# Kernel tuning notes

Measured on AMD Instinct MI355X. Metric: run time of the kernel, lower is better.

The kernel has to match this reference:

```python
import jax, jax.numpy as jnp
import numpy as np

B, S, D, H = 2, 2048, 1024, 16
DH = D // H
MASK_FACTOR = -10000.0
EPS = 1e-6


def setup_inputs() -> dict:
    key = jax.random.key(0)
    ks = jax.random.split(key, 12)
    sc = 1.0 / np.sqrt(D)
    inp = {
        'query': jax.random.normal(ks[0], (B, S, D), jnp.float32),
        'key':   jax.random.normal(ks[1], (B, S, D), jnp.float32),
        'value': jax.random.normal(ks[2], (B, S, D), jnp.float32),
        # mask: 1.0 = masked position (causal), shape (B, 1, Sq, Sk)
        'mask': jnp.broadcast_to(
            (1.0 - jnp.tril(jnp.ones((S, S), jnp.float32)))[None, None], (B, 1, S, S)
        ),
        'wq_w': jax.random.normal(ks[3], (D, D), jnp.float32) * sc,
        'wq_b': jnp.zeros((D,), jnp.float32),
        'wk_w': jax.random.normal(ks[4], (D, D), jnp.float32) * sc,
        'wk_b': jnp.zeros((D,), jnp.float32),
        'wv_w': jax.random.normal(ks[5], (D, D), jnp.float32) * sc,
        'wv_b': jnp.zeros((D,), jnp.float32),
        'wo_w': jax.random.normal(ks[6], (D, D), jnp.float32) * sc,
        'wo_b': jnp.zeros((D,), jnp.float32),
        'ln_g': jnp.ones((D,), jnp.float32),
        'ln_b': jnp.zeros((D,), jnp.float32),
    }
    return inp


def _split_heads(x):
    # (B, S, D) -> (B, H, S, DH)
    b, s, _ = x.shape
    return x.reshape(b, s, H, DH).transpose(0, 2, 1, 3)


def _layer_norm(x, g, b):
    mu = jnp.mean(x, axis=-1, keepdims=True)
    var = jnp.mean(jnp.square(x - mu), axis=-1, keepdims=True)
    return (x - mu) * jax.lax.rsqrt(var + EPS) * g + b


def reference(query, key, value, mask, wq_w, wq_b, wk_w, wk_b, wv_w, wv_b,
              wo_w, wo_b, ln_g, ln_b):
    q = _split_heads(query @ wq_w + wq_b)
    k = _split_heads(key @ wk_w + wk_b)
    v = _split_heads(value @ wv_w + wv_b)

    logits = jnp.einsum('bhqd,bhkd->bhqk', q, k) / jnp.sqrt(jnp.float32(DH))
    logits = logits * (1.0 - mask) + mask * MASK_FACTOR
    attn = jax.nn.softmax(logits, axis=-1)  # (B, H, Sq, Sk)

    ctx = jnp.einsum('bhqk,bhkd->bhqd', attn, v)
    ctx = ctx.transpose(0, 2, 1, 3).reshape(query.shape[0], -1, D)

    out = ctx @ wo_w + wo_b
    out = out + query  # residual
    out = _layer_norm(out, ln_g, ln_b)
    return out, attn
```

## Files before the change

kernel.cpp:

```cpp
#include <hip/hip_runtime.h>

#define B_ 2
#define S_ 2048
#define D_ 1024
#define H_ 16
#define DH_ 64
#define EPS_ 1e-6f

typedef short bf16x8 __attribute__((ext_vector_type(8)));
typedef float f32x4  __attribute__((ext_vector_type(4)));

__device__ __forceinline__ ushort f2bf(float x) {
    uint u = __float_as_uint(x);
    return (ushort)((u + 0x7fffu + ((u >> 16) & 1u)) >> 16);
}
__device__ __forceinline__ float bf2f(ushort h) {
    return __uint_as_float(((uint)h) << 16);
}
__device__ __forceinline__ void split_bf(float x, ushort& hi, ushort& lo) {
    hi = f2bf(x);
    lo = f2bf(x - bf2f(hi));
}

__global__ __launch_bounds__(256) void prep_weights_kernel(
    const float* __restrict__ w0, const float* __restrict__ w1,
    const float* __restrict__ w2, const float* __restrict__ w3,
    ushort* __restrict__ Wth, ushort* __restrict__ Wtl)
{
    const int wi = blockIdx.z;
    const float* W = (wi == 0) ? w0 : (wi == 1) ? w1 : (wi == 2) ? w2 : w3;
    ushort* th = Wth + (size_t)wi * D_ * D_;
    ushort* tl = Wtl + (size_t)wi * D_ * D_;
    const int k0 = blockIdx.x * 32, n0 = blockIdx.y * 32;
    const int tid = threadIdx.x;
    __shared__ float t[32][33];
#pragma unroll
    for (int l = 0; l < 4; ++l) {
        int idx = tid + l * 256;
        int kk = idx >> 5, nn = idx & 31;
        t[kk][nn] = W[(size_t)(k0 + kk) * D_ + n0 + nn];
    }
    __syncthreads();
#pragma unroll
    for (int l = 0; l < 4; ++l) {
        int idx = tid + l * 256;
        int nn = idx >> 5, kk = idx & 31;
        ushort h, lo;
        split_bf(t[kk][nn], h, lo);
        th[(size_t)(n0 + nn) * D_ + k0 + kk] = h;
        tl[(size_t)(n0 + nn) * D_ + k0 + kk] = lo;
    }
}

template <int MODE>
__device__ __forceinline__ void gemm_mfma_body(
    const float* __restrict__ A, const ushort* __restrict__ Bh,
    const ushort* __restrict__ Bl, const float* __restrict__ bias,
    const float* __restrict__ residual, float* __restrict__ Cf,
    ushort* __restrict__ Ch, ushort* __restrict__ Cl,
    int M, int N, int K, int bx, int by)
{
    __shared__ ushort Ah[128][40];
    __shared__ ushort Al[128][40];

    const int tid = threadIdx.x;
    const int lane = tid & 63, w = tid >> 6;
    const int l15 = lane & 15, l4 = lane >> 4;
    const int row0 = by * 128, col0 = bx * 128;
    const int wm = (w >> 1) * 64, wn = (w & 1) * 64;

    const f32x4 zf = {0.f, 0.f, 0.f, 0.f};
    f32x4 acc[4][4];
#pragma unroll
    for (int i = 0; i < 4; ++i)
#pragma unroll
        for (int j = 0; j < 4; ++j) acc[i][j] = zf;

    for (int k0 = 0; k0 < K; k0 += 32) {
#pragma unroll
        for (int l = 0; l < 4; ++l) {
            int idx = tid + l * 256;
            int r = idx >> 3, c4 = (idx & 7) * 4;
            const float4 a = *(const float4*)&A[(size_t)(row0 + r) * K + k0 + c4];
            ushort h0, h1, h2, h3, q0, q1, q2, q3;
            split_bf(a.x, h0, q0); split_bf(a.y, h1, q1);
            split_bf(a.z, h2, q2); split_bf(a.w, h3, q3);
            *(ushort4*)&Ah[r][c4] = make_ushort4(h0, h1, h2, h3);
            *(ushort4*)&Al[r][c4] = make_ushort4(q0, q1, q2, q3);
        }
        bf16x8 bh_[4], bl_[4];
#pragma unroll
        for (int j = 0; j < 4; ++j) {
            const size_t bo = (size_t)(col0 + wn + j * 16 + l15) * K + k0 + l4 * 8;
            bh_[j] = *(const bf16x8*)&Bh[bo];
            bl_[j] = *(const bf16x8*)&Bl[bo];
        }
        __syncthreads();
        bf16x8 ah_[4], al_[4];
#pragma unroll
        for (int i = 0; i < 4; ++i) {
            ah_[i] = *(const bf16x8*)&Ah[wm + i * 16 + l15][l4 * 8];
            al_[i] = *(const bf16x8*)&Al[wm + i * 16 + l15][l4 * 8];
        }
#pragma unroll
        for (int i = 0; i < 4; ++i)
#pragma unroll
            for (int j = 0; j < 4; ++j) {
                acc[i][j] = __builtin_amdgcn_mfma_f32_16x16x32_bf16(
                    ah_[i], bh_[j], acc[i][j], 0, 0, 0);
                acc[i][j] = __builtin_amdgcn_mfma_f32_16x16x32_bf16(
                    ah_[i], bl_[j], acc[i][j], 0, 0, 0);
                acc[i][j] = __builtin_amdgcn_mfma_f32_16x16x32_bf16(
                    al_[i], bh_[j], acc[i][j], 0, 0, 0);
            }
        __syncthreads();
    }

#pragma unroll
    for (int i = 0; i < 4; ++i) {
#pragma unroll
        for (int j = 0; j < 4; ++j) {
            const int col = col0 + wn + j * 16 + l15;
            const float bb = bias[col];
            const int mbase = row0 + wm + i * 16 + l4 * 4;
            if (MODE == 0) {
#pragma unroll
                for (int e = 0; e < 4; ++e) {
                    const int m = mbase + e;
                    float v = acc[i][j][e] + bb;
                    if (residual) v += residual[(size_t)m * N + col];
                    Cf[(size_t)m * N + col] = v;
                }
            } else if (MODE == 1) {
#pragma unroll
                for (int e = 0; e < 4; ++e) {
                    const int m = mbase + e;
                    ushort h, lo;
                    split_bf(acc[i][j][e] + bb, h, lo);
                    Ch[(size_t)m * N + col] = h;
                    Cl[(size_t)m * N + col] = lo;
                }
            } else {
                const int bb_ = mbase / S_;
                const int s0 = mbase - bb_ * S_;
                const int hh = col >> 6, dh = col & 63;
                ushort hv[4], lv[4];
#pragma unroll
                for (int e = 0; e < 4; ++e)
                    split_bf(acc[i][j][e] + bb, hv[e], lv[e]);
                const size_t ofs =
                    (((size_t)bb_ * H_ + hh) * DH_ + dh) * S_ + s0;
                *(ushort4*)&Ch[ofs] = make_ushort4(hv[0], hv[1], hv[2], hv[3]);
                *(ushort4*)&Cl[ofs] = make_ushort4(lv[0], lv[1], lv[2], lv[3]);
            }
        }
    }
}

__global__ __launch_bounds__(256) void gemm_qkv_mfma(
    const float* __restrict__ q, const float* __restrict__ k,
    const float* __restrict__ v,
    const ushort* __restrict__ Wth, const ushort* __restrict__ Wtl,
    const float* __restrict__ bq, const float* __restrict__ bk,
    const float* __restrict__ bv,
    ushort* __restrict__ Qh, ushort* __restrict__ Ql,
    ushort* __restrict__ Kh, ushort* __restrict__ Kl,
    ushort* __restrict__ Vth, ushort* __restrict__ Vtl)
{
    const int z = blockIdx.z;
    const size_t wofs = (size_t)z * D_ * D_;
    if (z == 0)
        gemm_mfma_body<1>(q, Wth, Wtl, bq, nullptr, nullptr, Qh, Ql,
                          B_ * S_, D_, D_, blockIdx.x, blockIdx.y);
    else if (z == 1)
        gemm_mfma_body<1>(k, Wth + wofs, Wtl + wofs, bk, nullptr, nullptr,
                          Kh, Kl, B_ * S_, D_, D_, blockIdx.x, blockIdx.y);
    else
        gemm_mfma_body<2>(v, Wth + wofs, Wtl + wofs, bv, nullptr, nullptr,
                          Vth, Vtl, B_ * S_, D_, D_, blockIdx.x, blockIdx.y);
}

__global__ __launch_bounds__(256) void gemm_out_mfma(
    const float* __restrict__ ctx, const ushort* __restrict__ Wth,
    const ushort* __restrict__ Wtl, const float* __restrict__ bias,
    const float* __restrict__ residual, float* __restrict__ pre)
{
    gemm_mfma_body<0>(ctx, Wth, Wtl, bias, residual, pre, nullptr, nullptr,
                      B_ * S_, D_, D_, blockIdx.x, blockIdx.y);
}

__global__ __launch_bounds__(256) void qk_mfma_kernel(
    const ushort* __restrict__ Qh, const ushort* __restrict__ Ql,
    const ushort* __restrict__ Kh, const ushort* __restrict__ Kl,
    float* __restrict__ logits)
{
    const int tk = blockIdx.x, tq = blockIdx.y;
    if (tk > tq) return;
    const int bh = blockIdx.z, b = bh >> 4, h = bh & 15;
    const int tid = threadIdx.x;
    const int lane = tid & 63, w = tid >> 6;
    const int l15 = lane & 15, l4 = lane >> 4;
    const int wm = (w >> 1) * 64, wn = (w & 1) * 64;

    const size_t qbase = ((size_t)b * S_ + tq * 128 + wm) * D_ + h * DH_;
    const size_t kbase = ((size_t)b * S_ + tk * 128 + wn) * D_ + h * DH_;

    const f32x4 zf = {0.f, 0.f, 0.f, 0.f};
    f32x4 acc[4][4];
#pragma unroll
    for (int i = 0; i < 4; ++i)
#pragma unroll
        for (int j = 0; j < 4; ++j) acc[i][j] = zf;

#pragma unroll
    for (int ks = 0; ks < 2; ++ks) {
        const int ko = ks * 32 + l4 * 8;
        bf16x8 ah_[4], al_[4], bh_[4], bl_[4];
#pragma unroll
        for (int i = 0; i < 4; ++i) {
            const size_t qo = qbase + (size_t)(i * 16 + l15) * D_ + ko;
            ah_[i] = *(const bf16x8*)&Qh[qo];
            al_[i] = *(const bf16x8*)&Ql[qo];
            const size_t kko = kbase + (size_t)(i * 16 + l15) * D_ + ko;
            bh_[i] = *(const bf16x8*)&Kh[kko];
            bl_[i] = *(const bf16x8*)&Kl[kko];
        }
#pragma unroll
        for (int i = 0; i < 4; ++i)
#pragma unroll
            for (int j = 0; j < 4; ++j) {
                acc[i][j] = __builtin_amdgcn_mfma_f32_16x16x32_bf16(
                    ah_[i], bh_[j], acc[i][j], 0, 0, 0);
                acc[i][j] = __builtin_amdgcn_mfma_f32_16x16x32_bf16(
                    ah_[i], bl_[j], acc[i][j], 0, 0, 0);
                acc[i][j] = __builtin_amdgcn_mfma_f32_16x16x32_bf16(
                    al_[i], bh_[j], acc[i][j], 0, 0, 0);
            }
    }

    float* out = logits + ((size_t)bh * S_ + tq * 128 + wm) * S_ + tk * 128 + wn;
#pragma unroll
    for (int i = 0; i < 4; ++i)
#pragma unroll
        for (int j = 0; j < 4; ++j) {
            const int col = j * 16 + l15;
#pragma unroll
            for (int e = 0; e < 4; ++e) {
                const int m = i * 16 + l4 * 4 + e;
                out[(size_t)m * S_ + col] = acc[i][j][e] * 0.125f;
            }
        }
}

__global__ __launch_bounds__(256) void softmax_kernel(float* __restrict__ attn)
{
    const int qi = blockIdx.x;
    const int bh = blockIdx.y;
    const int tid = threadIdx.x;
    const int lane = tid & 63, wid = tid >> 6;
    float* row = attn + ((size_t)bh * S_ + qi) * S_;
    const int len = qi + 1;
    const int len4 = (len + 3) >> 2;

    __shared__ float lg[S_];
    __shared__ float red[8];

    const float4* row4 = (const float4*)row;
    float lmax = -INFINITY;
    for (int j4 = tid; j4 < len4; j4 += 256) {
        float4 v = row4[j4];
        const int j = j4 * 4;
        if (j + 1 >= len) v.y = -INFINITY;
        if (j + 2 >= len) v.z = -INFINITY;
        if (j + 3 >= len) v.w = -INFINITY;
        *(float4*)&lg[j] = v;
        lmax = fmaxf(fmaxf(lmax, fmaxf(v.x, v.y)), fmaxf(v.z, v.w));
    }
#pragma unroll
    for (int o = 32; o > 0; o >>= 1) lmax = fmaxf(lmax, __shfl_xor(lmax, o));
    if (lane == 0) red[wid] = lmax;
    __syncthreads();
    const float m = fmaxf(fmaxf(red[0], red[1]), fmaxf(red[2], red[3]));

    float lsum = 0.f;
    for (int j = tid; j < len; j += 256) {
        float e = __expf(lg[j] - m);
        lg[j] = e;
        lsum += e;
    }
#pragma unroll
    for (int o = 32; o > 0; o >>= 1) lsum += __shfl_xor(lsum, o);
    if (lane == 0) red[4 + wid] = lsum;
    __syncthreads();
    const float inv = 1.f / (red[4] + red[5] + red[6] + red[7]);

    float4* wrow4 = (float4*)row;
    for (int j4 = tid; j4 < S_ / 4; j4 += 256) {
        const int j = j4 * 4;
        float4 o;
        o.x = (j     < len) ? lg[j]     * inv : 0.f;
        o.y = (j + 1 < len) ? lg[j + 1] * inv : 0.f;
        o.z = (j + 2 < len) ? lg[j + 2] * inv : 0.f;
        o.w = (j + 3 < len) ? lg[j + 3] * inv : 0.f;
        wrow4[j4] = o;
    }
}

__global__ __launch_bounds__(256) void pv_mfma_kernel(
    const float* __restrict__ P, const ushort* __restrict__ Vth,
    const ushort* __restrict__ Vtl, float* __restrict__ ctx)
{
    const int tq = blockIdx.x, bh = blockIdx.y, sp = blockIdx.z;
    if (sp > tq) return;
    const int b = bh >> 4, h = bh & 15;
    const int tid = threadIdx.x;
    const int lane = tid & 63, w = tid >> 6;
    const int l15 = lane & 15, l4 = lane >> 4;
    const int wm = w * 64;

    __shared__ ushort Ph[256][40];
    __shared__ ushort Pl[256][40];

    const float* Arow = P + ((size_t)bh * S_ + (size_t)tq * 256) * S_;
    const size_t vbase = ((size_t)b * H_ + h) * (size_t)DH_ * S_;

    const f32x4 zf = {0.f, 0.f, 0.f, 0.f};
    f32x4 acc[4][4];
#pragma unroll
    for (int i = 0; i < 4; ++i)
#pragma unroll
        for (int j = 0; j < 4; ++j) acc[i][j] = zf;

    const int kb = sp * 256;
    for (int k0 = kb; k0 < kb + 256; k0 += 32) {
#pragma unroll
        for (int l = 0; l < 8; ++l) {
            int idx = tid + l * 256;
            int r = idx >> 3, c4 = (idx & 7) * 4;
            const float4 a = *(const float4*)&Arow[(size_t)r * S_ + k0 + c4];
            ushort h0, h1, h2, h3, q0, q1, q2, q3;
            split_bf(a.x, h0, q0); split_bf(a.y, h1, q1);
            split_bf(a.z, h2, q2); split_bf(a.w, h3, q3);
            *(ushort4*)&Ph[r][c4] = make_ushort4(h0, h1, h2, h3);
            *(ushort4*)&Pl[r][c4] = make_ushort4(q0, q1, q2, q3);
        }
        bf16x8 bh_[4], bl_[4];
#pragma unroll
        for (int j = 0; j < 4; ++j) {
            const size_t vo = vbase + (size_t)(j * 16 + l15) * S_ + k0 + l4 * 8;
            bh_[j] = *(const bf16x8*)&Vth[vo];
            bl_[j] = *(const bf16x8*)&Vtl[vo];
        }
        __syncthreads();
        bf16x8 ah_[4], al_[4];
#pragma unroll
        for (int i = 0; i < 4; ++i) {
            ah_[i] = *(const bf16x8*)&Ph[wm + i * 16 + l15][l4 * 8];
            al_[i] = *(const bf16x8*)&Pl[wm + i * 16 + l15][l4 * 8];
        }
#pragma unroll
        for (int i = 0; i < 4; ++i)
#pragma unroll
            for (int j = 0; j < 4; ++j) {
                acc[i][j] = __builtin_amdgcn_mfma_f32_16x16x32_bf16(
                    ah_[i], bh_[j], acc[i][j], 0, 0, 0);
                acc[i][j] = __builtin_amdgcn_mfma_f32_16x16x32_bf16(
                    ah_[i], bl_[j], acc[i][j], 0, 0, 0);
                acc[i][j] = __builtin_amdgcn_mfma_f32_16x16x32_bf16(
                    al_[i], bh_[j], acc[i][j], 0, 0, 0);
            }
        __syncthreads();
    }

    float* C = ctx + ((size_t)b * S_ + (size_t)tq * 256 + wm) * D_ + h * DH_;
#pragma unroll
    for (int i = 0; i < 4; ++i)
#pragma unroll
        for (int j = 0; j < 4; ++j) {
            const int col = j * 16 + l15;
#pragma unroll
            for (int e = 0; e < 4; ++e) {
                const int m = i * 16 + l4 * 4 + e;
                atomicAdd(&C[(size_t)m * D_ + col], acc[i][j][e]);
            }
        }
}

__global__ __launch_bounds__(256) void ln_kernel(
    const float* __restrict__ X, const float* __restrict__ gamma,
    const float* __restrict__ beta, float* __restrict__ out)
{
    const int row = blockIdx.x;
    const int tid = threadIdx.x;
    const float* x = X + (size_t)row * D_;
    __shared__ float red[256];

    float s = 0.f;
    for (int i = tid; i < D_; i += 256) s += x[i];
    red[tid] = s;
    __syncthreads();
    for (int t = 128; t > 0; t >>= 1) {
        if (tid < t) red[tid] += red[tid + t];
        __syncthreads();
    }
    const float mu = red[0] * (1.f / D_);
    __syncthreads();

    float v = 0.f;
    for (int i = tid; i < D_; i += 256) {
        float t = x[i] - mu;
        v += t * t;
    }
    red[tid] = v;
    __syncthreads();
    for (int t = 128; t > 0; t >>= 1) {
        if (tid < t) red[tid] += red[tid + t];
        __syncthreads();
    }
    const float r = rsqrtf(red[0] * (1.f / D_) + EPS_);

    for (int i = tid; i < D_; i += 256) {
        float o = (x[i] - mu) * r * gamma[i] + beta[i];
        out[(size_t)row * D_ + i] = o;
    }
}

extern "C" void kernel_launch(void* const* d_in, const int* in_sizes, int n_in,
                              void* d_out, int out_size, void* d_ws, size_t ws_size,
                              hipStream_t stream)
{
    const float* query = (const float*)d_in[0];
    const float* key   = (const float*)d_in[1];
    const float* value = (const float*)d_in[2];
    const float* wq_w = (const float*)d_in[4];
    const float* wq_b = (const float*)d_in[5];
    const float* wk_w = (const float*)d_in[6];
    const float* wk_b = (const float*)d_in[7];
    const float* wv_w = (const float*)d_in[8];
    const float* wv_b = (const float*)d_in[9];
    const float* wo_w = (const float*)d_in[10];
    const float* wo_b = (const float*)d_in[11];
    const float* ln_g = (const float*)d_in[12];
    const float* ln_b = (const float*)d_in[13];

    float* out_f  = (float*)d_out;
    float* attn_f = out_f + (size_t)B_ * S_ * D_;

    const size_t NELEM = (size_t)B_ * S_ * D_;
    const size_t WELEM = (size_t)4 * D_ * D_;
    char* p = (char*)d_ws;
    ushort* Wth = (ushort*)p; p += WELEM * 2;
    ushort* Wtl = (ushort*)p; p += WELEM * 2;
    ushort* Qh  = (ushort*)p; p += NELEM * 2;
    ushort* Ql  = (ushort*)p; p += NELEM * 2;
    ushort* Kh  = (ushort*)p; p += NELEM * 2;
    ushort* Kl  = (ushort*)p; p += NELEM * 2;
    ushort* Vth = (ushort*)p; p += NELEM * 2;
    ushort* Vtl = (ushort*)p; p += NELEM * 2;
    float*  ctx = (float*)p;  p += NELEM * 4;
    float*  pre = (float*)p;  p += NELEM * 4;

    hipLaunchKernelGGL(prep_weights_kernel, dim3(D_ / 32, D_ / 32, 4), dim3(256),
                       0, stream, wq_w, wk_w, wv_w, wo_w, Wth, Wtl);

    hipLaunchKernelGGL(gemm_qkv_mfma, dim3(D_ / 128, (B_ * S_) / 128, 3),
                       dim3(256), 0, stream,
                       query, key, value, Wth, Wtl, wq_b, wk_b, wv_b,
                       Qh, Ql, Kh, Kl, Vth, Vtl);

    hipMemsetAsync(ctx, 0, NELEM * sizeof(float), stream);

    hipLaunchKernelGGL(qk_mfma_kernel, dim3(S_ / 128, S_ / 128, B_ * H_),
                       dim3(256), 0, stream, Qh, Ql, Kh, Kl, attn_f);

    hipLaunchKernelGGL(softmax_kernel, dim3(S_, B_ * H_), dim3(256), 0, stream,
                       attn_f);

    hipLaunchKernelGGL(pv_mfma_kernel, dim3(S_ / 256, B_ * H_, S_ / 256),
                       dim3(256), 0, stream, attn_f, Vth, Vtl, ctx);

    hipLaunchKernelGGL(gemm_out_mfma, dim3(D_ / 128, (B_ * S_) / 128),
                       dim3(256), 0, stream,
                       ctx, Wth + (size_t)3 * D_ * D_, Wtl + (size_t)3 * D_ * D_,
                       wo_b, query, pre);

    hipLaunchKernelGGL(ln_kernel, dim3(B_ * S_), dim3(256), 0, stream,
                       pre, ln_g, ln_b, out_f);
}
```

Measured before the change: 1.225 ms.

## Fuse QK^T logits and causal softmax into one LDS-resident strip kernel

Replaces the separate QK^T MFMA kernel and softmax kernel with one kernel. Each 1024-thread block computes a 16-row strip of logits into shared memory (about 128 KB), applies the causal softmax per row with one wave per row, and writes the normalized probabilities once. This drops the global write and re-read of the logits matrix and one kernel launch. In exchange the large LDS footprint allows only one block per CU, K fragments are reloaded from global memory for every 16-row strip with no tile reuse, and the 16-wide MFMA tiles have little data reuse.

```diff
diff --git a/kernel.cpp b/kernel.cpp
--- a/kernel.cpp
+++ b/kernel.cpp
@@ -189,120 +189,92 @@
                       B_ * S_, D_, D_, blockIdx.x, blockIdx.y);
 }
 
-__global__ __launch_bounds__(256) void qk_mfma_kernel(
+#define RS_ 2056
+
+__global__ __launch_bounds__(1024) void qksm_kernel(
     const ushort* __restrict__ Qh, const ushort* __restrict__ Ql,
     const ushort* __restrict__ Kh, const ushort* __restrict__ Kl,
-    float* __restrict__ logits)
-{
-    const int tk = blockIdx.x, tq = blockIdx.y;
-    if (tk > tq) return;
-    const int bh = blockIdx.z, b = bh >> 4, h = bh & 15;
+    float* __restrict__ attn)
+{
+    extern __shared__ float S_lds[];
+    const int bh = blockIdx.x;
+    const int strip = blockIdx.y;
+    const int b = bh >> 4, h = bh & 15;
+    const int s0 = strip * 16;
     const int tid = threadIdx.x;
-    const int lane = tid & 63, w = tid >> 6;
+    const int w = tid >> 6, lane = tid & 63;
     const int l15 = lane & 15, l4 = lane >> 4;
-    const int wm = (w >> 1) * 64, wn = (w & 1) * 64;
-
-    const size_t qbase = ((size_t)b * S_ + tq * 128 + wm) * D_ + h * DH_;
-    const size_t kbase = ((size_t)b * S_ + tk * 128 + wn) * D_ + h * DH_;
-
-    const f32x4 zf = {0.f, 0.f, 0.f, 0.f};
-    f32x4 acc[4][4];
-#pragma unroll
-    for (int i = 0; i < 4; ++i)
-#pragma unroll
-        for (int j = 0; j < 4; ++j) acc[i][j] = zf;
-
-#pragma unroll
-    for (int ks = 0; ks < 2; ++ks) {
-        const int ko = ks * 32 + l4 * 8;
-        bf16x8 ah_[4], al_[4], bh_[4], bl_[4];
-#pragma unroll
-        for (int i = 0; i < 4; ++i) {
-            const size_t qo = qbase + (size_t)(i * 16 + l15) * D_ + ko;
-            ah_[i] = *(const bf16x8*)&Qh[qo];
-            al_[i] = *(const bf16x8*)&Ql[qo];
-            const size_t kko = kbase + (size_t)(i * 16 + l15) * D_ + ko;
-            bh_[i] = *(const bf16x8*)&Kh[kko];
-            bl_[i] = *(const bf16x8*)&Kl[kko];
-        }
-#pragma unroll
-        for (int i = 0; i < 4; ++i)
-#pragma unroll
-            for (int j = 0; j < 4; ++j) {
-                acc[i][j] = __builtin_amdgcn_mfma_f32_16x16x32_bf16(
-                    ah_[i], bh_[j], acc[i][j], 0, 0, 0);
-                acc[i][j] = __builtin_amdgcn_mfma_f32_16x16x32_bf16(
-                    ah_[i], bl_[j], acc[i][j], 0, 0, 0);
-                acc[i][j] = __builtin_amdgcn_mfma_f32_16x16x32_bf16(
-                    al_[i], bh_[j], acc[i][j], 0, 0, 0);
-            }
-    }
-
-    float* out = logits + ((size_t)bh * S_ + tq * 128 + wm) * S_ + tk * 128 + wn;
-#pragma unroll
-    for (int i = 0; i < 4; ++i)
-#pragma unroll
-        for (int j = 0; j < 4; ++j) {
-            const int col = j * 16 + l15;
-#pragma unroll
-            for (int e = 0; e < 4; ++e) {
-                const int m = i * 16 + l4 * 4 + e;
-                out[(size_t)m * S_ + col] = acc[i][j][e] * 0.125f;
-            }
-        }
-}
-
-__global__ __launch_bounds__(256) void softmax_kernel(float* __restrict__ attn)
-{
-    const int qi = blockIdx.x;
-    const int bh = blockIdx.y;
-    const int tid = threadIdx.x;
-    const int lane = tid & 63, wid = tid >> 6;
-    float* row = attn + ((size_t)bh * S_ + qi) * S_;
+    const int lenmax = s0 + 16;
+
+    const size_t qbase = ((size_t)b * S_ + s0 + l15) * D_ + h * DH_ + l4 * 8;
+    const bf16x8 ah0 = *(const bf16x8*)&Qh[qbase];
+    const bf16x8 ah1 = *(const bf16x8*)&Qh[qbase + 32];
+    const bf16x8 al0 = *(const bf16x8*)&Ql[qbase];
+    const bf16x8 al1 = *(const bf16x8*)&Ql[qbase + 32];
+
+    for (int jf = 0; jf < 8; ++jf) {
+        const int k0 = w * 128 + jf * 16;
+        if (k0 >= lenmax) break;
+        const size_t kb = ((size_t)b * S_ + k0 + l15) * D_ + h * DH_ + l4 * 8;
+        const bf16x8 bh0 = *(const bf16x8*)&Kh[kb];
+        const bf16x8 bh1 = *(const bf16x8*)&Kh[kb + 32];
+        const bf16x8 bl0 = *(const bf16x8*)&Kl[kb];
+        const bf16x8 bl1 = *(const bf16x8*)&Kl[kb + 32];
+        f32x4 acc = {0.f, 0.f, 0.f, 0.f};
+        acc = __builtin_amdgcn_mfma_f32_16x16x32_bf16(ah0, bh0, acc, 0, 0, 0);
+        acc = __builtin_amdgcn_mfma_f32_16x16x32_bf16(ah0, bl0, acc, 0, 0, 0);
+        acc = __builtin_amdgcn_mfma_f32_16x16x32_bf16(al0, bh0, acc, 0, 0, 0);
+        acc = __builtin_amdgcn_mfma_f32_16x16x32_bf16(ah1, bh1, acc, 0, 0, 0);
+        acc = __builtin_amdgcn_mfma_f32_16x16x32_bf16(ah1, bl1, acc, 0, 0, 0);
+        acc = __builtin_amdgcn_mfma_f32_16x16x32_bf16(al1, bh1, acc, 0, 0, 0);
+#pragma unroll
+        for (int e = 0; e < 4; ++e)
+            S_lds[(l4 * 4 + e) * RS_ + k0 + l15] = acc[e] * 0.125f;
+    }
+    __syncthreads();
+
+    const int qi = s0 + w;
     const int len = qi + 1;
     const int len4 = (len + 3) >> 2;
-
-    __shared__ float lg[S_];
-    __shared__ float red[8];
-
-    const float4* row4 = (const float4*)row;
+    float* Srow = &S_lds[w * RS_];
+
     float lmax = -INFINITY;
-    for (int j4 = tid; j4 < len4; j4 += 256) {
-        float4 v = row4[j4];
+    for (int j4 = lane; j4 < len4; j4 += 64) {
+        float4 v = *(const float4*)&Srow[j4 * 4];
         const int j = j4 * 4;
         if (j + 1 >= len) v.y = -INFINITY;
         if (j + 2 >= len) v.z = -INFINITY;
         if (j + 3 >= len) v.w = -INFINITY;
-        *(float4*)&lg[j] = v;
         lmax = fmaxf(fmaxf(lmax, fmaxf(v.x, v.y)), fmaxf(v.z, v.w));
     }
 #pragma unroll
     for (int o = 32; o > 0; o >>= 1) lmax = fmaxf(lmax, __shfl_xor(lmax, o));
-    if (lane == 0) red[wid] = lmax;
-    __syncthreads();
-    const float m = fmaxf(fmaxf(red[0], red[1]), fmaxf(red[2], red[3]));
+    const float m = lmax;
 
     float lsum = 0.f;
-    for (int j = tid; j < len; j += 256) {
-        float e = __expf(lg[j] - m);
-        lg[j] = e;
-        lsum += e;
+    for (int j4 = lane; j4 < len4; j4 += 64) {
+        float4 v = *(float4*)&Srow[j4 * 4];
+        const int j = j4 * 4;
+        float4 e;
+        e.x = (j     < len) ? __expf(v.x - m) : 0.f;
+        e.y = (j + 1 < len) ? __expf(v.y - m) : 0.f;
+        e.z = (j + 2 < len) ? __expf(v.z - m) : 0.f;
+        e.w = (j + 3 < len) ? __expf(v.w - m) : 0.f;
+        *(float4*)&Srow[j4 * 4] = e;
+        lsum += e.x + e.y + e.z + e.w;
     }
 #pragma unroll
     for (int o = 32; o > 0; o >>= 1) lsum += __shfl_xor(lsum, o);
-    if (lane == 0) red[4 + wid] = lsum;
-    __syncthreads();
-    const float inv = 1.f / (red[4] + red[5] + red[6] + red[7]);
-
-    float4* wrow4 = (float4*)row;
-    for (int j4 = tid; j4 < S_ / 4; j4 += 256) {
-        const int j = j4 * 4;
-        float4 o;
-        o.x = (j     < len) ? lg[j]     * inv : 0.f;
-        o.y = (j + 1 < len) ? lg[j + 1] * inv : 0.f;
-        o.z = (j + 2 < len) ? lg[j + 2] * inv : 0.f;
-        o.w = (j + 3 < len) ? lg[j + 3] * inv : 0.f;
-        wrow4[j4] = o;
+    const float inv = 1.f / lsum;
+
+    float4* out4 = (float4*)(attn + ((size_t)bh * S_ + qi) * S_);
+    for (int j4 = lane; j4 < S_ / 4; j4 += 64) {
+        float4 o = {0.f, 0.f, 0.f, 0.f};
+        if (j4 < len4) {
+            const float4 e = *(const float4*)&Srow[j4 * 4];
+            o.x = e.x * inv; o.y = e.y * inv; o.z = e.z * inv; o.w = e.w * inv;
+        }
+        out4[j4] = o;
     }
 }
 
@@ -470,11 +442,9 @@
 
     hipMemsetAsync(ctx, 0, NELEM * sizeof(float), stream);
 
-    hipLaunchKernelGGL(qk_mfma_kernel, dim3(S_ / 128, S_ / 128, B_ * H_),
-                       dim3(256), 0, stream, Qh, Ql, Kh, Kl, attn_f);
-
-    hipLaunchKernelGGL(softmax_kernel, dim3(S_, B_ * H_), dim3(256), 0, stream,
-                       attn_f);
+    hipLaunchKernelGGL(qksm_kernel, dim3(B_ * H_, S_ / 16), dim3(1024),
+                       16 * RS_ * sizeof(float), stream,
+                       Qh, Ql, Kh, Kl, attn_f);
 
     hipLaunchKernelGGL(pv_mfma_kernel, dim3(S_ / 256, B_ * H_, S_ / 256),
                        dim3(256), 0, stream, attn_f, Vth, Vtl, ctx);
```

Result: faster. 1.147 ms (-6.3%).

## Replace QK/softmax/PV pipeline with flash attention plus attention-probability recompute kernel

Applied to the files above, without the earlier changes.

Fuses QK, causal softmax and PV into one flash-style kernel. It uses an online max/sum and keeps the context in split bf16 hi/lo form, which removes the atomics and the memset. A separate kernel recomputes the QK logits and writes the normalized attention matrix from the stored row max and inverse sum, and zero-fills the masked upper tiles. The intent is to avoid writing logits, re-reading them in the softmax pass and reading them again for PV, at the cost of computing QK twice. The flash kernel loads K and V from global memory per wave without sharing them through LDS, and its causal loop lengths are unbalanced across blocks.

```diff
diff --git a/kernel.cpp b/kernel.cpp
--- a/kernel.cpp
+++ b/kernel.cpp
@@ -9,6 +9,8 @@
 
 typedef short bf16x8 __attribute__((ext_vector_type(8)));
 typedef float f32x4  __attribute__((ext_vector_type(4)));
+
+#define MFMA16 __builtin_amdgcn_mfma_f32_16x16x32_bf16
 
 __device__ __forceinline__ ushort f2bf(float x) {
     uint u = __float_as_uint(x);
@@ -56,7 +58,6 @@
 __device__ __forceinline__ void gemm_mfma_body(
     const float* __restrict__ A, const ushort* __restrict__ Bh,
     const ushort* __restrict__ Bl, const float* __restrict__ bias,
-    const float* __restrict__ residual, float* __restrict__ Cf,
     ushort* __restrict__ Ch, ushort* __restrict__ Cl,
     int M, int N, int K, int bx, int by)
 {
@@ -106,12 +107,9 @@
         for (int i = 0; i < 4; ++i)
 #pragma unroll
             for (int j = 0; j < 4; ++j) {
-                acc[i][j] = __builtin_amdgcn_mfma_f32_16x16x32_bf16(
-                    ah_[i], bh_[j], acc[i][j], 0, 0, 0);
-                acc[i][j] = __builtin_amdgcn_mfma_f32_16x16x32_bf16(
-                    ah_[i], bl_[j], acc[i][j], 0, 0, 0);
-                acc[i][j] = __builtin_amdgcn_mfma_f32_16x16x32_bf16(
-                    al_[i], bh_[j], acc[i][j], 0, 0, 0);
+                acc[i][j] = MFMA16(ah_[i], bh_[j], acc[i][j], 0, 0, 0);
+                acc[i][j] = MFMA16(ah_[i], bl_[j], acc[i][j], 0, 0, 0);
+                acc[i][j] = MFMA16(al_[i], bh_[j], acc[i][j], 0, 0, 0);
             }
         __syncthreads();
     }
@@ -123,15 +121,7 @@
             const int col = col0 + wn + j * 16 + l15;
             const float bb = bias[col];
             const int mbase = row0 + wm + i * 16 + l4 * 4;
-            if (MODE == 0) {
-#pragma unroll
-                for (int e = 0; e < 4; ++e) {
-                    const int m = mbase + e;
-                    float v = acc[i][j][e] + bb;
-                    if (residual) v += residual[(size_t)m * N + col];
-                    Cf[(size_t)m * N + col] = v;
-                }
-            } else if (MODE == 1) {
+            if (MODE == 1) {
 #pragma unroll
                 for (int e = 0; e < 4; ++e) {
                     const int m = mbase + e;
@@ -170,40 +160,230 @@
     const int z = blockIdx.z;
     const size_t wofs = (size_t)z * D_ * D_;
     if (z == 0)
-        gemm_mfma_body<1>(q, Wth, Wtl, bq, nullptr, nullptr, Qh, Ql,
+        gemm_mfma_body<1>(q, Wth, Wtl, bq, Qh, Ql,
                           B_ * S_, D_, D_, blockIdx.x, blockIdx.y);
     else if (z == 1)
-        gemm_mfma_body<1>(k, Wth + wofs, Wtl + wofs, bk, nullptr, nullptr,
-                          Kh, Kl, B_ * S_, D_, D_, blockIdx.x, blockIdx.y);
+        gemm_mfma_body<1>(k, Wth + wofs, Wtl + wofs, bk, Kh, Kl,
+                          B_ * S_, D_, D_, blockIdx.x, blockIdx.y);
     else
-        gemm_mfma_body<2>(v, Wth + wofs, Wtl + wofs, bv, nullptr, nullptr,
-                          Vth, Vtl, B_ * S_, D_, D_, blockIdx.x, blockIdx.y);
-}
-
-__global__ __launch_bounds__(256) void gemm_out_mfma(
-    const float* __restrict__ ctx, const ushort* __restrict__ Wth,
-    const ushort* __restrict__ Wtl, const float* __restrict__ bias,
-    const float* __restrict__ residual, float* __restrict__ pre)
-{
-    gemm_mfma_body<0>(ctx, Wth, Wtl, bias, residual, pre, nullptr, nullptr,
-                      B_ * S_, D_, D_, blockIdx.x, blockIdx.y);
-}
-
-__global__ __launch_bounds__(256) void qk_mfma_kernel(
+        gemm_mfma_body<2>(v, Wth + wofs, Wtl + wofs, bv, Vth, Vtl,
+                          B_ * S_, D_, D_, blockIdx.x, blockIdx.y);
+}
+
+__global__ __launch_bounds__(256) void flash_kernel(
     const ushort* __restrict__ Qh, const ushort* __restrict__ Ql,
     const ushort* __restrict__ Kh, const ushort* __restrict__ Kl,
-    float* __restrict__ logits)
-{
-    const int tk = blockIdx.x, tq = blockIdx.y;
-    if (tk > tq) return;
-    const int bh = blockIdx.z, b = bh >> 4, h = bh & 15;
+    const ushort* __restrict__ Vth, const ushort* __restrict__ Vtl,
+    ushort* __restrict__ Ch, ushort* __restrict__ Cl,
+    float* __restrict__ Mrow, float* __restrict__ Irow)
+{
+    __shared__ ushort Pbh[4][16][40];
+    __shared__ ushort Pbl[4][16][40];
+    const int bh = blockIdx.x, qt = blockIdx.y;
+    const int b = bh >> 4, h = bh & 15;
+    const int tid = threadIdx.x;
+    const int w = tid >> 6, lane = tid & 63;
+    const int l15 = lane & 15, l4 = lane >> 4;
+    const int q0 = qt * 64 + w * 16;
+
+    const size_t qb = ((size_t)b * S_ + q0 + l15) * D_ + h * DH_ + l4 * 8;
+    const bf16x8 ah0 = *(const bf16x8*)&Qh[qb];
+    const bf16x8 ah1 = *(const bf16x8*)&Qh[qb + 32];
+    const bf16x8 al0 = *(const bf16x8*)&Ql[qb];
+    const bf16x8 al1 = *(const bf16x8*)&Ql[qb + 32];
+
+    const size_t vbase = ((size_t)b * H_ + h) * (size_t)DH_ * S_;
+
+    float m_run[4], l_run[4];
+#pragma unroll
+    for (int e = 0; e < 4; ++e) { m_run[e] = -INFINITY; l_run[e] = 0.f; }
+    const f32x4 zf = {0.f, 0.f, 0.f, 0.f};
+    f32x4 acc[4] = {zf, zf, zf, zf};
+
+    const int kmax = q0 + 16;
+    for (int kt = 0; kt < kmax; kt += 32) {
+        f32x4 s0, s1;
+#pragma unroll
+        for (int cf = 0; cf < 2; ++cf) {
+            const int kc0 = kt + cf * 16;
+            const size_t kb = ((size_t)b * S_ + kc0 + l15) * D_ + h * DH_ + l4 * 8;
+            const bf16x8 kh0 = *(const bf16x8*)&Kh[kb];
+            const bf16x8 kh1 = *(const bf16x8*)&Kh[kb + 32];
+            const bf16x8 kl0 = *(const bf16x8*)&Kl[kb];
+            const bf16x8 kl1 = *(const bf16x8*)&Kl[kb + 32];
+            f32x4 a = zf;
+            a = MFMA16(ah0, kh0, a, 0, 0, 0);
+            a = MFMA16(ah0, kl0, a, 0, 0, 0);
+            a = MFMA16(al0, kh0, a, 0, 0, 0);
+            a = MFMA16(ah1, kh1, a, 0, 0, 0);
+            a = MFMA16(ah1, kl1, a, 0, 0, 0);
+            a = MFMA16(al1, kh1, a, 0, 0, 0);
+            const int kk = kc0 + l15;
+            f32x4 sv;
+#pragma unroll
+            for (int e = 0; e < 4; ++e) {
+                const int qi = q0 + l4 * 4 + e;
+                sv[e] = (kk <= qi) ? a[e] * 0.125f : -INFINITY;
+            }
+            if (cf == 0) s0 = sv; else s1 = sv;
+        }
+        float p0[4], p1[4], f_[4];
+#pragma unroll
+        for (int e = 0; e < 4; ++e) {
+            float mx = fmaxf(s0[e], s1[e]);
+            mx = fmaxf(mx, __shfl_xor(mx, 1));
+            mx = fmaxf(mx, __shfl_xor(mx, 2));
+            mx = fmaxf(mx, __shfl_xor(mx, 4));
+            mx = fmaxf(mx, __shfl_xor(mx, 8));
+            const float mn = fmaxf(m_run[e], mx);
+            f_[e] = __expf(m_run[e] - mn);
+            m_run[e] = mn;
+            p0[e] = __expf(s0[e] - mn);
+            p1[e] = __expf(s1[e] - mn);
+            float sm = p0[e] + p1[e];
+            sm += __shfl_xor(sm, 1);
+            sm += __shfl_xor(sm, 2);
+            sm += __shfl_xor(sm, 4);
+            sm += __shfl_xor(sm, 8);
+            l_run[e] = l_run[e] * f_[e] + sm;
+        }
+#pragma unroll
+        for (int j = 0; j < 4; ++j)
+#pragma unroll
+            for (int e = 0; e < 4; ++e) acc[j][e] *= f_[e];
+#pragma unroll
+        for (int e = 0; e < 4; ++e) {
+            ushort hh, ll;
+            split_bf(p0[e], hh, ll);
+            Pbh[w][l4 * 4 + e][l15] = hh;
+            Pbl[w][l4 * 4 + e][l15] = ll;
+            split_bf(p1[e], hh, ll);
+            Pbh[w][l4 * 4 + e][16 + l15] = hh;
+            Pbl[w][l4 * 4 + e][16 + l15] = ll;
+        }
+        const bf16x8 pah = *(const bf16x8*)&Pbh[w][l15][l4 * 8];
+        const bf16x8 pal = *(const bf16x8*)&Pbl[w][l15][l4 * 8];
+#pragma unroll
+        for (int j = 0; j < 4; ++j) {
+            const size_t vo = vbase + (size_t)(j * 16 + l15) * S_ + kt + l4 * 8;
+            const bf16x8 vh = *(const bf16x8*)&Vth[vo];
+            const bf16x8 vl = *(const bf16x8*)&Vtl[vo];
+            acc[j] = MFMA16(pah, vh, acc[j], 0, 0, 0);
+            acc[j] = MFMA16(pah, vl, acc[j], 0, 0, 0);
+            acc[j] = MFMA16(pal, vh, acc[j], 0, 0, 0);
+        }
+    }
+    float inv[4];
+#pragma unroll
+    for (int e = 0; e < 4; ++e) inv[e] = 1.f / l_run[e];
+#pragma unroll
+    for (int j = 0; j < 4; ++j)
+#pragma unroll
+        for (int e = 0; e < 4; ++e) {
+            const size_t mo = ((size_t)b * S_ + q0 + l4 * 4 + e) * D_
+                              + h * DH_ + j * 16 + l15;
+            ushort hh, ll;
+            split_bf(acc[j][e] * inv[e], hh, ll);
+            Ch[mo] = hh; Cl[mo] = ll;
+        }
+    if (l15 == 0) {
+#pragma unroll
+        for (int e = 0; e < 4; ++e) {
+            Mrow[(size_t)bh * S_ + q0 + l4 * 4 + e] = m_run[e];
+            Irow[(size_t)bh * S_ + q0 + l4 * 4 + e] = inv[e];
+        }
+    }
+}
+
+__global__ __launch_bounds__(256) void attn_write_kernel(
+    const ushort* __restrict__ Qh, const ushort* __restrict__ Ql,
+    const ushort* __restrict__ Kh, const ushort* __restrict__ Kl,
+    const float* __restrict__ Mrow, const float* __restrict__ Irow,
+    float* __restrict__ attn)
+{
+    const int tk = blockIdx.x, tq = blockIdx.y, bh = blockIdx.z;
+    const int tid = threadIdx.x;
+    if (tk > tq) {
+        const float4 z = {0.f, 0.f, 0.f, 0.f};
+        for (int idx = tid; idx < 128 * 32; idx += 256) {
+            const int r = idx >> 5, c = idx & 31;
+            *(float4*)&attn[((size_t)bh * S_ + tq * 128 + r) * S_
+                            + tk * 128 + c * 4] = z;
+        }
+        return;
+    }
+    const int b = bh >> 4, h = bh & 15;
+    const int lane = tid & 63, w = tid >> 6;
+    const int l15 = lane & 15, l4 = lane >> 4;
+    const int wm = (w >> 1) * 64, wn = (w & 1) * 64;
+
+    const size_t qbase = ((size_t)b * S_ + tq * 128 + wm) * D_ + h * DH_;
+    const size_t kbase = ((size_t)b * S_ + tk * 128 + wn) * D_ + h * DH_;
+
+    const f32x4 zf = {0.f, 0.f, 0.f, 0.f};
+    f32x4 acc[4][4];
+#pragma unroll
+    for (int i = 0; i < 4; ++i)
+#pragma unroll
+        for (int j = 0; j < 4; ++j) acc[i][j] = zf;
+
+#pragma unroll
+    for (int ks = 0; ks < 2; ++ks) {
+        const int ko = ks * 32 + l4 * 8;
+        bf16x8 qh_[4], ql_[4], kh_[4], kl_[4];
+#pragma unroll
+        for (int i = 0; i < 4; ++i) {
+            const size_t qo = qbase + (size_t)(i * 16 + l15) * D_ + ko;
+            qh_[i] = *(const bf16x8*)&Qh[qo];
+            ql_[i] = *(const bf16x8*)&Ql[qo];
+            const size_t kko = kbase + (size_t)(i * 16 + l15) * D_ + ko;
+            kh_[i] = *(const bf16x8*)&Kh[kko];
+            kl_[i] = *(const bf16x8*)&Kl[kko];
+        }
+#pragma unroll
+        for (int i = 0; i < 4; ++i)
+#pragma unroll
+            for (int j = 0; j < 4; ++j) {
+                acc[i][j] = MFMA16(qh_[i], kh_[j], acc[i][j], 0, 0, 0);
+                acc[i][j] = MFMA16(qh_[i], kl_[j], acc[i][j], 0, 0, 0);
+                acc[i][j] = MFMA16(ql_[i], kh_[j], acc[i][j], 0, 0, 0);
+            }
+    }
+
+#pragma unroll
+    for (int i = 0; i < 4; ++i) {
+        float mi[4], ii[4];
+        int qi_[4];
+#pragma unroll
+        for (int e = 0; e < 4; ++e) {
+            qi_[e] = tq * 128 + wm + i * 16 + l4 * 4 + e;
+            mi[e] = Mrow[(size_t)bh * S_ + qi_[e]];
+            ii[e] = Irow[(size_t)bh * S_ + qi_[e]];
+        }
+#pragma unroll
+        for (int j = 0; j < 4; ++j) {
+            const int kk = tk * 128 + wn + j * 16 + l15;
+#pragma unroll
+            for (int e = 0; e < 4; ++e) {
+                const float val = (kk <= qi_[e])
+                    ? __expf(acc[i][j][e] * 0.125f - mi[e]) * ii[e] : 0.f;
+                attn[((size_t)bh * S_ + qi_[e]) * S_ + kk] = val;
+            }
+        }
+    }
+}
+
+__global__ __launch_bounds__(256) void gemm_out2_kernel(
+    const ushort* __restrict__ Ah, const ushort* __restrict__ Al,
+    const ushort* __restrict__ Bh, const ushort* __restrict__ Bl,
+    const float* __restrict__ bias, const float* __restrict__ residual,
+    float* __restrict__ out)
+{
     const int tid = threadIdx.x;
     const int lane = tid & 63, w = tid >> 6;
     const int l15 = lane & 15, l4 = lane >> 4;
+    const int row0 = blockIdx.y * 128, col0 = blockIdx.x * 128;
     const int wm = (w >> 1) * 64, wn = (w & 1) * 64;
-
-    const size_t qbase = ((size_t)b * S_ + tq * 128 + wm) * D_ + h * DH_;
-    const size_t kbase = ((size_t)b * S_ + tk * 128 + wn) * D_ + h * DH_;
 
     const f32x4 zf = {0.f, 0.f, 0.f, 0.f};
     f32x4 acc[4][4];
@@ -212,176 +392,38 @@
 #pragma unroll
         for (int j = 0; j < 4; ++j) acc[i][j] = zf;
 
-#pragma unroll
-    for (int ks = 0; ks < 2; ++ks) {
-        const int ko = ks * 32 + l4 * 8;
+    for (int k0 = 0; k0 < D_; k0 += 32) {
         bf16x8 ah_[4], al_[4], bh_[4], bl_[4];
 #pragma unroll
         for (int i = 0; i < 4; ++i) {
-            const size_t qo = qbase + (size_t)(i * 16 + l15) * D_ + ko;
-            ah_[i] = *(const bf16x8*)&Qh[qo];
-            al_[i] = *(const bf16x8*)&Ql[qo];
-            const size_t kko = kbase + (size_t)(i * 16 + l15) * D_ + ko;
-            bh_[i] = *(const bf16x8*)&Kh[kko];
-            bl_[i] = *(const bf16x8*)&Kl[kko];
+            const size_t ao = (size_t)(row0 + wm + i * 16 + l15) * D_ + k0 + l4 * 8;
+            ah_[i] = *(const bf16x8*)&Ah[ao];
+            al_[i] = *(const bf16x8*)&Al[ao];
+            const size_t bo = (size_t)(col0 + wn + i * 16 + l15) * D_ + k0 + l4 * 8;
+            bh_[i] = *(const bf16x8*)&Bh[bo];
+            bl_[i] = *(const bf16x8*)&Bl[bo];
         }
 #pragma unroll
         for (int i = 0; i < 4; ++i)
 #pragma unroll
             for (int j = 0; j < 4; ++j) {
-                acc[i][j] = __builtin_amdgcn_mfma_f32_16x16x32_bf16(
-                    ah_[i], bh_[j], acc[i][j], 0, 0, 0);
-                acc[i][j] = __builtin_amdgcn_mfma_f32_16x16x32_bf16(
-                    ah_[i], bl_[j], acc[i][j], 0, 0, 0);
-                acc[i][j] = __builtin_amdgcn_mfma_f32_16x16x32_bf16(
-                    al_[i], bh_[j], acc[i][j], 0, 0, 0);
-            }
-    }
-
-    float* out = logits + ((size_t)bh * S_ + tq * 128 + wm) * S_ + tk * 128 + wn;
+                acc[i][j] = MFMA16(ah_[i], bh_[j], acc[i][j], 0, 0, 0);
+                acc[i][j] = MFMA16(ah_[i], bl_[j], acc[i][j], 0, 0, 0);
+                acc[i][j] = MFMA16(al_[i], bh_[j], acc[i][j], 0, 0, 0);
+            }
+    }
+
 #pragma unroll
     for (int i = 0; i < 4; ++i)
 #pragma unroll
         for (int j = 0; j < 4; ++j) {
-            const int col = j * 16 + l15;
+            const int col = col0 + wn + j * 16 + l15;
+            const float bb = bias[col];
 #pragma unroll
             for (int e = 0; e < 4; ++e) {
-                const int m = i * 16 + l4 * 4 + e;
-                out[(size_t)m * S_ + col] = acc[i][j][e] * 0.125f;
-            }
-        }
-}
-
-__global__ __launch_bounds__(256) void softmax_kernel(float* __restrict__ attn)
-{
-    const int qi = blockIdx.x;
-    const int bh = blockIdx.y;
-    const int tid = threadIdx.x;
-    const int lane = tid & 63, wid = tid >> 6;
-    float* row = attn + ((size_t)bh * S_ + qi) * S_;
-    const int len = qi + 1;
-    const int len4 = (len + 3) >> 2;
-
-    __shared__ float lg[S_];
-    __shared__ float red[8];
-
-    const float4* row4 = (const float4*)row;
-    float lmax = -INFINITY;
-    for (int j4 = tid; j4 < len4; j4 += 256) {
-        float4 v = row4[j4];
-        const int j = j4 * 4;
-        if (j + 1 >= len) v.y = -INFINITY;
-        if (j + 2 >= len) v.z = -INFINITY;
-        if (j + 3 >= len) v.w = -INFINITY;
-        *(float4*)&lg[j] = v;
-        lmax = fmaxf(fmaxf(lmax, fmaxf(v.x, v.y)), fmaxf(v.z, v.w));
-    }
-#pragma unroll
-    for (int o = 32; o > 0; o >>= 1) lmax = fmaxf(lmax, __shfl_xor(lmax, o));
-    if (lane == 0) red[wid] = lmax;
-    __syncthreads();
-    const float m = fmaxf(fmaxf(red[0], red[1]), fmaxf(red[2], red[3]));
-
-    float lsum = 0.f;
-    for (int j = tid; j < len; j += 256) {
-        float e = __expf(lg[j] - m);
-        lg[j] = e;
-        lsum += e;
-    }
-#pragma unroll
-    for (int o = 32; o > 0; o >>= 1) lsum += __shfl_xor(lsum, o);
-    if (lane == 0) red[4 + wid] = lsum;
-    __syncthreads();
-    const float inv = 1.f / (red[4] + red[5] + red[6] + red[7]);
-
-    float4* wrow4 = (float4*)row;
-    for (int j4 = tid; j4 < S_ / 4; j4 += 256) {
-        const int j = j4 * 4;
-        float4 o;
-        o.x = (j     < len) ? lg[j]     * inv : 0.f;
-        o.y = (j + 1 < len) ? lg[j + 1] * inv : 0.f;
-        o.z = (j + 2 < len) ? lg[j + 2] * inv : 0.f;
-        o.w = (j + 3 < len) ? lg[j + 3] * inv : 0.f;
-        wrow4[j4] = o;
-    }
-}
-
-__global__ __launch_bounds__(256) void pv_mfma_kernel(
-    const float* __restrict__ P, const ushort* __restrict__ Vth,
-    const ushort* __restrict__ Vtl, float* __restrict__ ctx)
-{
-    const int tq = blockIdx.x, bh = blockIdx.y, sp = blockIdx.z;
-    if (sp > tq) return;
-    const int b = bh >> 4, h = bh & 15;
-    const int tid = threadIdx.x;
-    const int lane = tid & 63, w = tid >> 6;
-    const int l15 = lane & 15, l4 = lane >> 4;
-    const int wm = w * 64;
-
-    __shared__ ushort Ph[256][40];
-    __shared__ ushort Pl[256][40];
-
-    const float* Arow = P + ((size_t)bh * S_ + (size_t)tq * 256) * S_;
-    const size_t vbase = ((size_t)b * H_ + h) * (size_t)DH_ * S_;
-
-    const f32x4 zf = {0.f, 0.f, 0.f, 0.f};
-    f32x4 acc[4][4];
-#pragma unroll
-    for (int i = 0; i < 4; ++i)
-#pragma unroll
-        for (int j = 0; j < 4; ++j) acc[i][j] = zf;
-
-    const int kb = sp * 256;
-    for (int k0 = kb; k0 < kb + 256; k0 += 32) {
-#pragma unroll
-        for (int l = 0; l < 8; ++l) {
-            int idx = tid + l * 256;
-            int r = idx >> 3, c4 = (idx & 7) * 4;
-            const float4 a = *(const float4*)&Arow[(size_t)r * S_ + k0 + c4];
-            ushort h0, h1, h2, h3, q0, q1, q2, q3;
-            split_bf(a.x, h0, q0); split_bf(a.y, h1, q1);
-            split_bf(a.z, h2, q2); split_bf(a.w, h3, q3);
-            *(ushort4*)&Ph[r][c4] = make_ushort4(h0, h1, h2, h3);
-            *(ushort4*)&Pl[r][c4] = make_ushort4(q0, q1, q2, q3);
-        }
-        bf16x8 bh_[4], bl_[4];
-#pragma unroll
-        for (int j = 0; j < 4; ++j) {
-            const size_t vo = vbase + (size_t)(j * 16 + l15) * S_ + k0 + l4 * 8;
-            bh_[j] = *(const bf16x8*)&Vth[vo];
-            bl_[j] = *(const bf16x8*)&Vtl[vo];
-        }
-        __syncthreads();
-        bf16x8 ah_[4], al_[4];
-#pragma unroll
-        for (int i = 0; i < 4; ++i) {
-            ah_[i] = *(const bf16x8*)&Ph[wm + i * 16 + l15][l4 * 8];
-            al_[i] = *(const bf16x8*)&Pl[wm + i * 16 + l15][l4 * 8];
-        }
-#pragma unroll
-        for (int i = 0; i < 4; ++i)
-#pragma unroll
-            for (int j = 0; j < 4; ++j) {
-                acc[i][j] = __builtin_amdgcn_mfma_f32_16x16x32_bf16(
-                    ah_[i], bh_[j], acc[i][j], 0, 0, 0);
-                acc[i][j] = __builtin_amdgcn_mfma_f32_16x16x32_bf16(
-                    ah_[i], bl_[j], acc[i][j], 0, 0, 0);
-                acc[i][j] = __builtin_amdgcn_mfma_f32_16x16x32_bf16(
-                    al_[i], bh_[j], acc[i][j], 0, 0, 0);
-            }
-        __syncthreads();
-    }
-
-    float* C = ctx + ((size_t)b * S_ + (size_t)tq * 256 + wm) * D_ + h * DH_;
-#pragma unroll
-    for (int i = 0; i < 4; ++i)
-#pragma unroll
-        for (int j = 0; j < 4; ++j) {
-            const int col = j * 16 + l15;
-#pragma unroll
-            for (int e = 0; e < 4; ++e) {
-                const int m = i * 16 + l4 * 4 + e;
-                atomicAdd(&C[(size_t)m * D_ + col], acc[i][j][e]);
+                const int m = row0 + wm + i * 16 + l4 * 4 + e;
+                out[(size_t)m * D_ + col] =
+                    acc[i][j][e] + bb + residual[(size_t)m * D_ + col];
             }
         }
 }
@@ -449,16 +491,19 @@
     const size_t NELEM = (size_t)B_ * S_ * D_;
     const size_t WELEM = (size_t)4 * D_ * D_;
     char* p = (char*)d_ws;
-    ushort* Wth = (ushort*)p; p += WELEM * 2;
-    ushort* Wtl = (ushort*)p; p += WELEM * 2;
-    ushort* Qh  = (ushort*)p; p += NELEM * 2;
-    ushort* Ql  = (ushort*)p; p += NELEM * 2;
-    ushort* Kh  = (ushort*)p; p += NELEM * 2;
-    ushort* Kl  = (ushort*)p; p += NELEM * 2;
-    ushort* Vth = (ushort*)p; p += NELEM * 2;
-    ushort* Vtl = (ushort*)p; p += NELEM * 2;
-    float*  ctx = (float*)p;  p += NELEM * 4;
-    float*  pre = (float*)p;  p += NELEM * 4;
+    ushort* Wth  = (ushort*)p; p += WELEM * 2;
+    ushort* Wtl  = (ushort*)p; p += WELEM * 2;
+    ushort* Qh   = (ushort*)p; p += NELEM * 2;
+    ushort* Ql   = (ushort*)p; p += NELEM * 2;
+    ushort* Kh   = (ushort*)p; p += NELEM * 2;
+    ushort* Kl   = (ushort*)p; p += NELEM * 2;
+    ushort* Vth  = (ushort*)p; p += NELEM * 2;
+    ushort* Vtl  = (ushort*)p; p += NELEM * 2;
+    ushort* Ctxh = (ushort*)p; p += NELEM * 2;
+    ushort* Ctxl = (ushort*)p; p += NELEM * 2;
+    float*  pre  = (float*)p;  p += NELEM * 4;
+    float* Mrow = pre;
+    float* Irow = pre + (size_t)B_ * H_ * S_;
 
     hipLaunchKernelGGL(prep_weights_kernel, dim3(D_ / 32, D_ / 32, 4), dim3(256),
                        0, stream, wq_w, wk_w, wv_w, wo_w, Wth, Wtl);
@@ -468,21 +513,18 @@
                        query, key, value, Wth, Wtl, wq_b, wk_b, wv_b,
                        Qh, Ql, Kh, Kl, Vth, Vtl);
 
-    hipMemsetAsync(ctx, 0, NELEM * sizeof(float), stream);
-
-    hipLaunchKernelGGL(qk_mfma_kernel, dim3(S_ / 128, S_ / 128, B_ * H_),
-                       dim3(256), 0, stream, Qh, Ql, Kh, Kl, attn_f);
-
-    hipLaunchKernelGGL(softmax_kernel, dim3(S_, B_ * H_), dim3(256), 0, stream,
-                       attn_f);
-
-    hipLaunchKernelGGL(pv_mfma_kernel, dim3(S_ / 256, B_ * H_, S_ / 256),
-                       dim3(256), 0, stream, attn_f, Vth, Vtl, ctx);
-
-    hipLaunchKernelGGL(gemm_out_mfma, dim3(D_ / 128, (B_ * S_) / 128),
+    hipLaunchKernelGGL(flash_kernel, dim3(B_ * H_, S_ / 64), dim3(256),
+                       0, stream, Qh, Ql, Kh, Kl, Vth, Vtl,
+                       Ctxh, Ctxl, Mrow, Irow);
+
+    hipLaunchKernelGGL(attn_write_kernel, dim3(S_ / 128, S_ / 128, B_ * H_),
                        dim3(256), 0, stream,
-                       ctx, Wth + (size_t)3 * D_ * D_, Wtl + (size_t)3 * D_ * D_,
-                       wo_b, query, pre);
+                       Qh, Ql, Kh, Kl, Mrow, Irow, attn_f);
+
+    hipLaunchKernelGGL(gemm_out2_kernel, dim3(D_ / 128, (B_ * S_) / 128),
+                       dim3(256), 0, stream,
+                       Ctxh, Ctxl, Wth + (size_t)3 * D_ * D_,
+                       Wtl + (size_t)3 * D_ * D_, wo_b, query, pre);
 
     hipLaunchKernelGGL(ln_kernel, dim3(B_ * S_), dim3(256), 0, stream,
                        pre, ln_g, ln_b, out_f);
```

Measured after the change: 1.232 ms. Within noise of the previous version (+0.5%).
